# Kernel optimization log

Hardware: AMD Instinct MI355X
Metric: run time of the kernel (lower is better)

Reference implementation:

```python
import jax, jax.numpy as jnp
import numpy as np

B, N, OBS, ACT = 4, 256, 40, 8
HEAD, DIM = 8, 32
T = HEAD * DIM


def setup_inputs() -> dict:
    key = jax.random.key(0)
    ks = jax.random.split(key, 10)
    x = jax.random.normal(ks[0], (B, N + 1, OBS), dtype=jnp.float32)
    # last row, col 0 carries the (float-encoded) target intersection index
    tgt = jax.random.randint(ks[1], (B,), 0, N)
    x = x.at[:, -1, 0].set(tgt.astype(jnp.float32))
    adj = jax.random.uniform(ks[2], (N, N), dtype=jnp.float32)
    s = 0.02
    return {
        "x": x,
        "adj": adj,
        "We1": jax.random.normal(ks[3], (OBS, T), dtype=jnp.float32) * s,
        "be1": jnp.zeros((T,), jnp.float32),
        "We2": jax.random.normal(ks[4], (T, T), dtype=jnp.float32) * s,
        "be2": jnp.zeros((T,), jnp.float32),
        "Wl": jax.random.normal(ks[5], (T, T), dtype=jnp.float32) * s,
        "bl": jnp.zeros((T,), jnp.float32),
        "Wn": jax.random.normal(ks[6], (T, T), dtype=jnp.float32) * s,
        "bn": jnp.zeros((T,), jnp.float32),
        "Wh": jax.random.normal(ks[7], (T, T), dtype=jnp.float32) * s,
        "bh": jnp.zeros((T,), jnp.float32),
        "Wa": jax.random.normal(ks[8], (DIM, ACT), dtype=jnp.float32) * s,
        "ba": jnp.zeros((ACT,), jnp.float32),
    }


def reference(x, adj, We1, be1, We2, be2, Wl, bl, Wn, bn, Wh, bh, Wa, ba):
    b, np1, _ = x.shape
    n = np1 - 1
    tgt = x[:, -1, 0].astype(jnp.int32)          # [B] target intersection ids
    obs = x[:, :-1, :]                            # [B,N,OBS]
    # obs_embed: Linear+ReLU twice
    emb = jax.nn.relu(obs @ We1 + be1)
    emb = jax.nn.relu(emb @ We2 + be2)            # [B,N,T]
    # tile then matmul by adjacency: result is adj @ emb, replicated along dim 1
    ne = jnp.einsum('mn,bnd->bmd', adj, emb)      # [B,N,T]
    ne = jnp.broadcast_to(ne[:, None], (b, n, n, T))  # [B,N,N,T] (tiled, as in torch)
    # agent heads: [B,N,H,1,D]
    ah = jax.nn.relu(emb @ Wl + bl).reshape(b, n, 1, DIM, HEAD).transpose(0, 1, 4, 2, 3)
    # neighbor heads: [B,N,H,N,D]
    nh = jax.nn.relu(ne @ Wn + bn).reshape(b, n, n, DIM, HEAD).transpose(0, 1, 4, 2, 3)
    # einsum 'ijklm,ijknm->ijklm' with l=1: elementwise over d, summed over n
    attn = ah * nh.sum(axis=3, keepdims=True)     # [B,N,H,1,D]
    attn = jax.nn.softmax(attn, axis=-1)
    hid = jax.nn.relu(ne @ Wh + bh).reshape(b, n, n, DIM, HEAD).transpose(0, 1, 4, 2, 3)
    out = attn * hid.sum(axis=3, keepdims=True)   # [B,N,H,1,D]
    out = out.mean(axis=2).reshape(b, n, DIM)     # mean over heads -> [B,N,D]
    g = out[jnp.arange(b), tgt]                   # gather per-batch target row [B,D]
    act = g @ Wa + ba                             # [B,ACT]
    return act
```

## Files before the change

### kernel.cpp

```cpp
#include <hip/hip_runtime.h>

#define Bsz 4
#define Nn  256
#define OBSD 40
#define ACTD 8
#define HEADS 8
#define DIMD 32
#define Td  256
#define R   4

#define FMA4(accr, s, wv) \
    (accr).x = fmaf((s), (wv).x, (accr).x); \
    (accr).y = fmaf((s), (wv).y, (accr).y); \
    (accr).z = fmaf((s), (wv).z, (accr).z); \
    (accr).w = fmaf((s), (wv).w, (accr).w)

__global__ void k_emb(const float* __restrict__ x,
                      const float* __restrict__ We1, const float* __restrict__ be1,
                      const float* __restrict__ We2, const float* __restrict__ be2,
                      float* __restrict__ emb,
                      float* __restrict__ snh, float* __restrict__ shid,
                      unsigned* __restrict__ ctr) {
    int g = blockIdx.x;
    int t = threadIdx.x;
    int row0 = g * R;
    int b = row0 >> 8;
    int n0 = row0 & 255;
    if (g == 0)      { for (int i = t; i < Bsz * Td; i += 256) snh[i]  = 0.f; }
    else if (g == 1) { for (int i = t; i < Bsz * Td; i += 256) shid[i] = 0.f; }
    else if (g == 2) { if (t < Bsz) ctr[t] = 0u; }

    __shared__ float4 obs_t[OBSD];
    __shared__ float4 h1_t[Td];
    __shared__ float4 part[4][R][64];
    if (t < R * OBSD) {
        int r = t & (R - 1), k = t >> 2;
        ((float*)&obs_t[k])[r] = x[(b * (Nn + 1) + n0 + r) * OBSD + k];
    }
    __syncthreads();

    float bias1 = be1[t];
    float a1[R] = {bias1, bias1, bias1, bias1};
#pragma unroll
    for (int k = 0; k < OBSD; ++k) {
        float w = We1[k * Td + t];
        float4 ov = obs_t[k];
        a1[0] = fmaf(ov.x, w, a1[0]);
        a1[1] = fmaf(ov.y, w, a1[1]);
        a1[2] = fmaf(ov.z, w, a1[2]);
        a1[3] = fmaf(ov.w, w, a1[3]);
    }
    h1_t[t] = make_float4(fmaxf(a1[0], 0.f), fmaxf(a1[1], 0.f),
                          fmaxf(a1[2], 0.f), fmaxf(a1[3], 0.f));
    __syncthreads();

    int wv = t >> 6, c = t & 63;
    float4 a2[R] = {};
#pragma unroll 8
    for (int i = 0; i < 64; ++i) {
        int k = (wv << 6) + i;
        float4 wvv = *(const float4*)(We2 + k * Td + 4 * c);
        float4 hv = h1_t[k];
        FMA4(a2[0], hv.x, wvv);
        FMA4(a2[1], hv.y, wvv);
        FMA4(a2[2], hv.z, wvv);
        FMA4(a2[3], hv.w, wvv);
    }
#pragma unroll
    for (int r = 0; r < R; ++r) part[wv][r][c] = a2[r];
    __syncthreads();

    int c2 = t >> 2, j = t & 3;
#pragma unroll
    for (int r = 0; r < R; ++r) {
        float v = be2[t];
#pragma unroll
        for (int w2 = 0; w2 < 4; ++w2) v += ((const float*)&part[w2][r][c2])[j];
        emb[(row0 + r) * Td + t] = fmaxf(v, 0.f);
    }
}

__global__ void k_fused(const float* __restrict__ x,
                        const float* __restrict__ adj, const float* __restrict__ emb,
                        const float* __restrict__ Wn, const float* __restrict__ bn,
                        const float* __restrict__ Wh, const float* __restrict__ bh,
                        const float* __restrict__ Wl, const float* __restrict__ bl,
                        const float* __restrict__ Wa, const float* __restrict__ ba,
                        float* __restrict__ snh, float* __restrict__ shid,
                        unsigned* __restrict__ ctr,
                        float* __restrict__ out) {
    int g = blockIdx.x, b = blockIdx.y;
    int t = threadIdx.x;
    int m0 = g * R;
    __shared__ float4 arow_t[Nn];
    __shared__ float4 nrow_t[Td];
    __shared__ float4 partN[4][R][64];
    __shared__ float4 partH[4][R][64];
    arow_t[t] = make_float4(adj[(m0 + 0) * Nn + t], adj[(m0 + 1) * Nn + t],
                            adj[(m0 + 2) * Nn + t], adj[(m0 + 3) * Nn + t]);
    __syncthreads();

    int wv = t >> 6, c = t & 63;
    int c2 = t >> 2, j = t & 3;
    const float* eb = emb + b * Nn * Td;

    {
        float4 aN[R] = {};
#pragma unroll 8
        for (int i = 0; i < 64; ++i) {
            int n = (wv << 6) + i;
            float4 ev = *(const float4*)(eb + n * Td + 4 * c);
            float4 ar = arow_t[n];
            FMA4(aN[0], ar.x, ev);
            FMA4(aN[1], ar.y, ev);
            FMA4(aN[2], ar.z, ev);
            FMA4(aN[3], ar.w, ev);
        }
#pragma unroll
        for (int r = 0; r < R; ++r) partN[wv][r][c] = aN[r];
    }
    __syncthreads();
    {
        float nr[R];
#pragma unroll
        for (int r = 0; r < R; ++r) {
            float v = 0.f;
#pragma unroll
            for (int w2 = 0; w2 < 4; ++w2) v += ((const float*)&partN[w2][r][c2])[j];
            nr[r] = v;
        }
        nrow_t[t] = make_float4(nr[0], nr[1], nr[2], nr[3]);
    }
    __syncthreads();

    {
        float4 sN[R] = {};
        float4 sH[R] = {};
#pragma unroll 8
        for (int i = 0; i < 64; ++i) {
            int k = (wv << 6) + i;
            float4 nv = nrow_t[k];
            float4 wn4 = *(const float4*)(Wn + k * Td + 4 * c);
            float4 wh4 = *(const float4*)(Wh + k * Td + 4 * c);
            FMA4(sN[0], nv.x, wn4);  FMA4(sH[0], nv.x, wh4);
            FMA4(sN[1], nv.y, wn4);  FMA4(sH[1], nv.y, wh4);
            FMA4(sN[2], nv.z, wn4);  FMA4(sH[2], nv.z, wh4);
            FMA4(sN[3], nv.w, wn4);  FMA4(sH[3], nv.w, wh4);
        }
#pragma unroll
        for (int r = 0; r < R; ++r) { partN[wv][r][c] = sN[r]; partH[wv][r][c] = sH[r]; }
    }
    __syncthreads();

    {
        float bnt = bn[t], bht = bh[t];
        float rs1 = 0.f, rs2 = 0.f;
#pragma unroll
        for (int r = 0; r < R; ++r) {
            float v1 = bnt, v2 = bht;
#pragma unroll
            for (int w2 = 0; w2 < 4; ++w2) {
                v1 += ((const float*)&partN[w2][r][c2])[j];
                v2 += ((const float*)&partH[w2][r][c2])[j];
            }
            rs1 += fmaxf(v1, 0.f);
            rs2 += fmaxf(v2, 0.f);
        }
        atomicAdd(&snh[b * Td + t], rs1);
        atomicAdd(&shid[b * Td + t], rs2);
    }

    __shared__ int isLast;
    __threadfence();
    __syncthreads();
    if (t == 0) {
        unsigned old = __hip_atomic_fetch_add(&ctr[b], 1u, __ATOMIC_ACQ_REL,
                                              __HIP_MEMORY_SCOPE_AGENT);
        isLast = (old == (unsigned)(Nn / R - 1));
    }
    __syncthreads();
    if (!isLast) return;
    __threadfence();

    __shared__ float erow[Td], lg[Td], p[Td], od[DIMD];
    __shared__ float4 partL[4][64];
    int tgt = (int)x[(b * (Nn + 1) + Nn) * OBSD + 0];
    tgt = tgt < 0 ? 0 : (tgt > Nn - 1 ? Nn - 1 : tgt);
    erow[t] = emb[(b * Nn + tgt) * Td + t];
    __syncthreads();

    float4 aL = {};
#pragma unroll 8
    for (int i = 0; i < 64; ++i) {
        int k = (wv << 6) + i;
        float4 wlv = *(const float4*)(Wl + k * Td + 4 * c);
        FMA4(aL, erow[k], wlv);
    }
    partL[wv][c] = aL;
    __syncthreads();

    float acc = bl[t];
#pragma unroll
    for (int w2 = 0; w2 < 4; ++w2) acc += ((const float*)&partL[w2][c2])[j];
    float ah = fmaxf(acc, 0.f);
    lg[t] = ah * snh[b * Td + t];
    __syncthreads();
    int h = t & 7;
    float mx = -1e30f;
#pragma unroll
    for (int d = 0; d < DIMD; ++d) mx = fmaxf(mx, lg[d * HEADS + h]);
    float se = 0.f;
#pragma unroll
    for (int d = 0; d < DIMD; ++d) se += __expf(lg[d * HEADS + h] - mx);
    float attn = __expf(lg[t] - mx) / se;
    p[t] = attn * shid[b * Td + t];
    __syncthreads();
    if (t < DIMD) {
        float s = 0.f;
#pragma unroll
        for (int hh = 0; hh < HEADS; ++hh) s += p[t * HEADS + hh];
        od[t] = s * (1.f / HEADS);
    }
    __syncthreads();
    if (t < ACTD) {
        float s = ba[t];
#pragma unroll
        for (int d = 0; d < DIMD; ++d) s = fmaf(od[d], Wa[d * ACTD + t], s);
        out[b * ACTD + t] = s;
    }
}

extern "C" void kernel_launch(void* const* d_in, const int* in_sizes, int n_in,
                              void* d_out, int out_size, void* d_ws, size_t ws_size,
                              hipStream_t stream) {
    const float* x   = (const float*)d_in[0];
    const float* adj = (const float*)d_in[1];
    const float* We1 = (const float*)d_in[2];
    const float* be1 = (const float*)d_in[3];
    const float* We2 = (const float*)d_in[4];
    const float* be2 = (const float*)d_in[5];
    const float* Wl  = (const float*)d_in[6];
    const float* bl  = (const float*)d_in[7];
    const float* Wn  = (const float*)d_in[8];
    const float* bn  = (const float*)d_in[9];
    const float* Wh  = (const float*)d_in[10];
    const float* bh  = (const float*)d_in[11];
    const float* Wa  = (const float*)d_in[12];
    const float* ba  = (const float*)d_in[13];
    float* out = (float*)d_out;

    float* emb  = (float*)d_ws;
    float* snh  = emb + Bsz * Nn * Td;
    float* shid = snh + Bsz * Td;
    unsigned* ctr = (unsigned*)(shid + Bsz * Td);

    k_emb<<<dim3(Bsz * Nn / R), dim3(Td), 0, stream>>>(x, We1, be1, We2, be2,
                                                       emb, snh, shid, ctr);
    k_fused<<<dim3(Nn / R, Bsz), dim3(Td), 0, stream>>>(x, adj, emb, Wn, bn, Wh, bh,
                                                        Wl, bl, Wa, ba,
                                                        snh, shid, ctr, out);
}
```

Measured before the change: 125.0 us.

## Merge embed and fused kernels into one cooperative kernel with grid syncs

Replaces the two-kernel pipeline with one cooperative kernel of 256 blocks of 512 threads, using grid.sync between the embedding, adjacency/projection and final attention stages. The last-block atomic counter is dropped, and a fixed set of 4 blocks now runs the tail. Block size doubles, so each reduction over k is split across 8 waves instead of 4, halving the per-thread loop length. The aim is to remove the second launch and the counter handshake, at the price of grid-wide barrier cost, a cooperative launch requirement, and idle threads in the t<256 sections.

```diff
diff --git a/kernel.cpp b/kernel.cpp
--- a/kernel.cpp
+++ b/kernel.cpp
@@ -1,4 +1,7 @@
 #include <hip/hip_runtime.h>
+#include <hip/hip_cooperative_groups.h>
+
+namespace cg = cooperative_groups;
 
 #define Bsz 4
 #define Nn  256
@@ -7,7 +10,6 @@
 #define HEADS 8
 #define DIMD 32
 #define Td  256
-#define R   4
 
 #define FMA4(accr, s, wv) \
     (accr).x = fmaf((s), (wv).x, (accr).x); \
@@ -15,131 +17,126 @@
     (accr).z = fmaf((s), (wv).z, (accr).z); \
     (accr).w = fmaf((s), (wv).w, (accr).w)
 
-__global__ void k_emb(const float* __restrict__ x,
-                      const float* __restrict__ We1, const float* __restrict__ be1,
-                      const float* __restrict__ We2, const float* __restrict__ be2,
-                      float* __restrict__ emb,
-                      float* __restrict__ snh, float* __restrict__ shid,
-                      unsigned* __restrict__ ctr) {
-    int g = blockIdx.x;
+__global__ __launch_bounds__(512) void k_one(
+        const float* __restrict__ x,   const float* __restrict__ adj,
+        const float* __restrict__ We1, const float* __restrict__ be1,
+        const float* __restrict__ We2, const float* __restrict__ be2,
+        const float* __restrict__ Wl,  const float* __restrict__ bl,
+        const float* __restrict__ Wn,  const float* __restrict__ bn,
+        const float* __restrict__ Wh,  const float* __restrict__ bh,
+        const float* __restrict__ Wa,  const float* __restrict__ ba,
+        float* __restrict__ emb, float* __restrict__ snh,
+        float* __restrict__ shid, float* __restrict__ out) {
+    cg::grid_group grid = cg::this_grid();
+    int bid = blockIdx.x;
     int t = threadIdx.x;
-    int row0 = g * R;
-    int b = row0 >> 8;
-    int n0 = row0 & 255;
-    if (g == 0)      { for (int i = t; i < Bsz * Td; i += 256) snh[i]  = 0.f; }
-    else if (g == 1) { for (int i = t; i < Bsz * Td; i += 256) shid[i] = 0.f; }
-    else if (g == 2) { if (t < Bsz) ctr[t] = 0u; }
-
-    __shared__ float4 obs_t[OBSD];
-    __shared__ float4 h1_t[Td];
-    __shared__ float4 part[4][R][64];
-    if (t < R * OBSD) {
-        int r = t & (R - 1), k = t >> 2;
-        ((float*)&obs_t[k])[r] = x[(b * (Nn + 1) + n0 + r) * OBSD + k];
+    int wv = t >> 6;
+    int c  = t & 63;
+    int c2 = (t & 255) >> 2, j = t & 3;
+
+    __shared__ float4 partN[8][4][64];
+    __shared__ float4 partH[8][4][64];
+    __shared__ float4 vecA[Nn];
+    __shared__ float4 vecB[Nn];
+    __shared__ float4 obs_s[OBSD];
+
+    {
+        int row0 = bid * 4;
+        int b = row0 >> 8, n0 = row0 & 255;
+        if (bid == 0)      { for (int i = t; i < Bsz * Td; i += 512) snh[i]  = 0.f; }
+        else if (bid == 1) { for (int i = t; i < Bsz * Td; i += 512) shid[i] = 0.f; }
+        if (t < 4 * OBSD) {
+            int r = t & 3, k = t >> 2;
+            ((float*)&obs_s[k])[r] = x[(b * (Nn + 1) + n0 + r) * OBSD + k];
+        }
+        __syncthreads();
+
+        if (t < Td) {
+            float bias1 = be1[t];
+            float a1[4] = {bias1, bias1, bias1, bias1};
+#pragma unroll
+            for (int k = 0; k < OBSD; ++k) {
+                float w = We1[k * Td + t];
+                float4 ov = obs_s[k];
+                a1[0] = fmaf(ov.x, w, a1[0]);
+                a1[1] = fmaf(ov.y, w, a1[1]);
+                a1[2] = fmaf(ov.z, w, a1[2]);
+                a1[3] = fmaf(ov.w, w, a1[3]);
+            }
+            vecB[t] = make_float4(fmaxf(a1[0], 0.f), fmaxf(a1[1], 0.f),
+                                  fmaxf(a1[2], 0.f), fmaxf(a1[3], 0.f));
+        }
+        __syncthreads();
+
+        float4 a2[4] = {};
+#pragma unroll 8
+        for (int i = 0; i < 32; ++i) {
+            int k = (wv << 5) + i;
+            float4 wvv = *(const float4*)(We2 + k * Td + 4 * c);
+            float4 hv = vecB[k];
+            FMA4(a2[0], hv.x, wvv);
+            FMA4(a2[1], hv.y, wvv);
+            FMA4(a2[2], hv.z, wvv);
+            FMA4(a2[3], hv.w, wvv);
+        }
+#pragma unroll
+        for (int r = 0; r < 4; ++r) partN[wv][r][c] = a2[r];
+        __syncthreads();
+
+        if (t < Td) {
+#pragma unroll
+            for (int r = 0; r < 4; ++r) {
+                float v = be2[t];
+#pragma unroll
+                for (int w = 0; w < 8; ++w) v += ((const float*)&partN[w][r][c2])[j];
+                emb[(row0 + r) * Td + t] = fmaxf(v, 0.f);
+            }
+        }
     }
-    __syncthreads();
-
-    float bias1 = be1[t];
-    float a1[R] = {bias1, bias1, bias1, bias1};
-#pragma unroll
-    for (int k = 0; k < OBSD; ++k) {
-        float w = We1[k * Td + t];
-        float4 ov = obs_t[k];
-        a1[0] = fmaf(ov.x, w, a1[0]);
-        a1[1] = fmaf(ov.y, w, a1[1]);
-        a1[2] = fmaf(ov.z, w, a1[2]);
-        a1[3] = fmaf(ov.w, w, a1[3]);
-    }
-    h1_t[t] = make_float4(fmaxf(a1[0], 0.f), fmaxf(a1[1], 0.f),
-                          fmaxf(a1[2], 0.f), fmaxf(a1[3], 0.f));
-    __syncthreads();
-
-    int wv = t >> 6, c = t & 63;
-    float4 a2[R] = {};
-#pragma unroll 8
-    for (int i = 0; i < 64; ++i) {
-        int k = (wv << 6) + i;
-        float4 wvv = *(const float4*)(We2 + k * Td + 4 * c);
-        float4 hv = h1_t[k];
-        FMA4(a2[0], hv.x, wvv);
-        FMA4(a2[1], hv.y, wvv);
-        FMA4(a2[2], hv.z, wvv);
-        FMA4(a2[3], hv.w, wvv);
-    }
-#pragma unroll
-    for (int r = 0; r < R; ++r) part[wv][r][c] = a2[r];
-    __syncthreads();
-
-    int c2 = t >> 2, j = t & 3;
-#pragma unroll
-    for (int r = 0; r < R; ++r) {
-        float v = be2[t];
-#pragma unroll
-        for (int w2 = 0; w2 < 4; ++w2) v += ((const float*)&part[w2][r][c2])[j];
-        emb[(row0 + r) * Td + t] = fmaxf(v, 0.f);
-    }
-}
-
-__global__ void k_fused(const float* __restrict__ x,
-                        const float* __restrict__ adj, const float* __restrict__ emb,
-                        const float* __restrict__ Wn, const float* __restrict__ bn,
-                        const float* __restrict__ Wh, const float* __restrict__ bh,
-                        const float* __restrict__ Wl, const float* __restrict__ bl,
-                        const float* __restrict__ Wa, const float* __restrict__ ba,
-                        float* __restrict__ snh, float* __restrict__ shid,
-                        unsigned* __restrict__ ctr,
-                        float* __restrict__ out) {
-    int g = blockIdx.x, b = blockIdx.y;
-    int t = threadIdx.x;
-    int m0 = g * R;
-    __shared__ float4 arow_t[Nn];
-    __shared__ float4 nrow_t[Td];
-    __shared__ float4 partN[4][R][64];
-    __shared__ float4 partH[4][R][64];
-    arow_t[t] = make_float4(adj[(m0 + 0) * Nn + t], adj[(m0 + 1) * Nn + t],
-                            adj[(m0 + 2) * Nn + t], adj[(m0 + 3) * Nn + t]);
-    __syncthreads();
-
-    int wv = t >> 6, c = t & 63;
-    int c2 = t >> 2, j = t & 3;
-    const float* eb = emb + b * Nn * Td;
+    grid.sync();
 
     {
-        float4 aN[R] = {};
-#pragma unroll 8
-        for (int i = 0; i < 64; ++i) {
-            int n = (wv << 6) + i;
+        int b = bid >> 6, m0 = (bid & 63) * 4;
+        const float* eb = emb + b * Nn * Td;
+        if (t < Td)
+            vecA[t] = make_float4(adj[(m0 + 0) * Nn + t], adj[(m0 + 1) * Nn + t],
+                                  adj[(m0 + 2) * Nn + t], adj[(m0 + 3) * Nn + t]);
+        __syncthreads();
+
+        float4 aN[4] = {};
+#pragma unroll 8
+        for (int i = 0; i < 32; ++i) {
+            int n = (wv << 5) + i;
             float4 ev = *(const float4*)(eb + n * Td + 4 * c);
-            float4 ar = arow_t[n];
+            float4 ar = vecA[n];
             FMA4(aN[0], ar.x, ev);
             FMA4(aN[1], ar.y, ev);
             FMA4(aN[2], ar.z, ev);
             FMA4(aN[3], ar.w, ev);
         }
 #pragma unroll
-        for (int r = 0; r < R; ++r) partN[wv][r][c] = aN[r];
-    }
-    __syncthreads();
-    {
-        float nr[R];
-#pragma unroll
-        for (int r = 0; r < R; ++r) {
-            float v = 0.f;
-#pragma unroll
-            for (int w2 = 0; w2 < 4; ++w2) v += ((const float*)&partN[w2][r][c2])[j];
-            nr[r] = v;
-        }
-        nrow_t[t] = make_float4(nr[0], nr[1], nr[2], nr[3]);
-    }
-    __syncthreads();
-
-    {
-        float4 sN[R] = {};
-        float4 sH[R] = {};
-#pragma unroll 8
-        for (int i = 0; i < 64; ++i) {
-            int k = (wv << 6) + i;
-            float4 nv = nrow_t[k];
+        for (int r = 0; r < 4; ++r) partN[wv][r][c] = aN[r];
+        __syncthreads();
+
+        if (t < Td) {
+            float nr[4];
+#pragma unroll
+            for (int r = 0; r < 4; ++r) {
+                float v = 0.f;
+#pragma unroll
+                for (int w = 0; w < 8; ++w) v += ((const float*)&partN[w][r][c2])[j];
+                nr[r] = v;
+            }
+            vecB[t] = make_float4(nr[0], nr[1], nr[2], nr[3]);
+        }
+        __syncthreads();
+
+        float4 sN[4] = {};
+        float4 sH[4] = {};
+#pragma unroll 8
+        for (int i = 0; i < 32; ++i) {
+            int k = (wv << 5) + i;
+            float4 nv = vecB[k];
             float4 wn4 = *(const float4*)(Wn + k * Td + 4 * c);
             float4 wh4 = *(const float4*)(Wh + k * Td + 4 * c);
             FMA4(sN[0], nv.x, wn4);  FMA4(sH[0], nv.x, wh4);
@@ -148,85 +145,81 @@
             FMA4(sN[3], nv.w, wn4);  FMA4(sH[3], nv.w, wh4);
         }
 #pragma unroll
-        for (int r = 0; r < R; ++r) { partN[wv][r][c] = sN[r]; partH[wv][r][c] = sH[r]; }
+        for (int r = 0; r < 4; ++r) { partN[wv][r][c] = sN[r]; partH[wv][r][c] = sH[r]; }
+        __syncthreads();
+
+        if (t < Td) {
+            float bnt = bn[t], bht = bh[t];
+            float rs1 = 0.f, rs2 = 0.f;
+#pragma unroll
+            for (int r = 0; r < 4; ++r) {
+                float v1 = bnt, v2 = bht;
+#pragma unroll
+                for (int w = 0; w < 8; ++w) {
+                    v1 += ((const float*)&partN[w][r][c2])[j];
+                    v2 += ((const float*)&partH[w][r][c2])[j];
+                }
+                rs1 += fmaxf(v1, 0.f);
+                rs2 += fmaxf(v2, 0.f);
+            }
+            atomicAdd(&snh[b * Td + t], rs1);
+            atomicAdd(&shid[b * Td + t], rs2);
+        }
     }
-    __syncthreads();
-
-    {
-        float bnt = bn[t], bht = bh[t];
-        float rs1 = 0.f, rs2 = 0.f;
-#pragma unroll
-        for (int r = 0; r < R; ++r) {
-            float v1 = bnt, v2 = bht;
-#pragma unroll
-            for (int w2 = 0; w2 < 4; ++w2) {
-                v1 += ((const float*)&partN[w2][r][c2])[j];
-                v2 += ((const float*)&partH[w2][r][c2])[j];
-            }
-            rs1 += fmaxf(v1, 0.f);
-            rs2 += fmaxf(v2, 0.f);
-        }
-        atomicAdd(&snh[b * Td + t], rs1);
-        atomicAdd(&shid[b * Td + t], rs2);
-    }
-
-    __shared__ int isLast;
-    __threadfence();
-    __syncthreads();
-    if (t == 0) {
-        unsigned old = __hip_atomic_fetch_add(&ctr[b], 1u, __ATOMIC_ACQ_REL,
-                                              __HIP_MEMORY_SCOPE_AGENT);
-        isLast = (old == (unsigned)(Nn / R - 1));
-    }
-    __syncthreads();
-    if (!isLast) return;
-    __threadfence();
-
-    __shared__ float erow[Td], lg[Td], p[Td], od[DIMD];
-    __shared__ float4 partL[4][64];
-    int tgt = (int)x[(b * (Nn + 1) + Nn) * OBSD + 0];
-    tgt = tgt < 0 ? 0 : (tgt > Nn - 1 ? Nn - 1 : tgt);
-    erow[t] = emb[(b * Nn + tgt) * Td + t];
-    __syncthreads();
-
-    float4 aL = {};
-#pragma unroll 8
-    for (int i = 0; i < 64; ++i) {
-        int k = (wv << 6) + i;
-        float4 wlv = *(const float4*)(Wl + k * Td + 4 * c);
-        FMA4(aL, erow[k], wlv);
-    }
-    partL[wv][c] = aL;
-    __syncthreads();
-
-    float acc = bl[t];
-#pragma unroll
-    for (int w2 = 0; w2 < 4; ++w2) acc += ((const float*)&partL[w2][c2])[j];
-    float ah = fmaxf(acc, 0.f);
-    lg[t] = ah * snh[b * Td + t];
-    __syncthreads();
-    int h = t & 7;
-    float mx = -1e30f;
-#pragma unroll
-    for (int d = 0; d < DIMD; ++d) mx = fmaxf(mx, lg[d * HEADS + h]);
-    float se = 0.f;
-#pragma unroll
-    for (int d = 0; d < DIMD; ++d) se += __expf(lg[d * HEADS + h] - mx);
-    float attn = __expf(lg[t] - mx) / se;
-    p[t] = attn * shid[b * Td + t];
-    __syncthreads();
-    if (t < DIMD) {
-        float s = 0.f;
-#pragma unroll
-        for (int hh = 0; hh < HEADS; ++hh) s += p[t * HEADS + hh];
-        od[t] = s * (1.f / HEADS);
-    }
-    __syncthreads();
-    if (t < ACTD) {
-        float s = ba[t];
-#pragma unroll
-        for (int d = 0; d < DIMD; ++d) s = fmaf(od[d], Wa[d * ACTD + t], s);
-        out[b * ACTD + t] = s;
+    grid.sync();
+
+    if (bid < Bsz) {
+        int b = bid;
+        float* erow = (float*)vecA;
+        float* lg   = (float*)vecB;
+        float* p    = (float*)vecB + Td;
+        float* od   = (float*)vecB + 2 * Td;
+        int tgt = (int)x[(b * (Nn + 1) + Nn) * OBSD + 0];
+        tgt = tgt < 0 ? 0 : (tgt > Nn - 1 ? Nn - 1 : tgt);
+        if (t < Td) erow[t] = emb[(b * Nn + tgt) * Td + t];
+        __syncthreads();
+
+        float4 aL = {};
+#pragma unroll 8
+        for (int i = 0; i < 32; ++i) {
+            int k = (wv << 5) + i;
+            float4 wlv = *(const float4*)(Wl + k * Td + 4 * c);
+            FMA4(aL, erow[k], wlv);
+        }
+        partN[wv][0][c] = aL;
+        __syncthreads();
+
+        if (t < Td) {
+            float acc = bl[t];
+#pragma unroll
+            for (int w = 0; w < 8; ++w) acc += ((const float*)&partN[w][0][c2])[j];
+            lg[t] = fmaxf(acc, 0.f) * snh[b * Td + t];
+        }
+        __syncthreads();
+        if (t < Td) {
+            int h = t & 7;
+            float mx = -1e30f;
+#pragma unroll
+            for (int d = 0; d < DIMD; ++d) mx = fmaxf(mx, lg[d * HEADS + h]);
+            float se = 0.f;
+#pragma unroll
+            for (int d = 0; d < DIMD; ++d) se += __expf(lg[d * HEADS + h] - mx);
+            p[t] = (__expf(lg[t] - mx) / se) * shid[b * Td + t];
+        }
+        __syncthreads();
+        if (t < DIMD) {
+            float s = 0.f;
+#pragma unroll
+            for (int hh = 0; hh < HEADS; ++hh) s += p[t * HEADS + hh];
+            od[t] = s * (1.f / HEADS);
+        }
+        __syncthreads();
+        if (t < ACTD) {
+            float s = ba[t];
+#pragma unroll
+            for (int d = 0; d < DIMD; ++d) s = fmaf(od[d], Wa[d * ACTD + t], s);
+            out[b * ACTD + t] = s;
+        }
     }
 }
 
@@ -252,11 +245,9 @@
     float* emb  = (float*)d_ws;
     float* snh  = emb + Bsz * Nn * Td;
     float* shid = snh + Bsz * Td;
-    unsigned* ctr = (unsigned*)(shid + Bsz * Td);
-
-    k_emb<<<dim3(Bsz * Nn / R), dim3(Td), 0, stream>>>(x, We1, be1, We2, be2,
-                                                       emb, snh, shid, ctr);
-    k_fused<<<dim3(Nn / R, Bsz), dim3(Td), 0, stream>>>(x, adj, emb, Wn, bn, Wh, bh,
-                                                        Wl, bl, Wa, ba,
-                                                        snh, shid, ctr, out);
+
+    void* args[] = {&x, &adj, &We1, &be1, &We2, &be2, &Wl, &bl, &Wn, &bn,
+                    &Wh, &bh, &Wa, &ba, &emb, &snh, &shid, &out};
+    hipLaunchCooperativeKernel((void*)k_one, dim3(Bsz * Nn / 4), dim3(512),
+                               args, 0, stream);
 }
```

Result: slower. 178.3 us (+42.6%).
